# Kernel tuning notes

Hardware: AMD Instinct MI355X
Metric: run time of the kernel (lower is better)

The kernel has to match this reference:

```python
import jax, jax.numpy as jnp
import numpy as np

OBS, ACT, H, O, B = 256, 64, 1024, 8, 4096
ALPHA, GAMMA, ACT_LIMIT = 0.2, 0.99, 1.0
LOG_STD_MIN, LOG_STD_MAX = -20.0, 2.0
D = OBS + ACT + O  # intra-Q input dim


def setup_inputs() -> dict:
    key = jax.random.key(0)
    ks = iter(jax.random.split(key, 64))
    w = lambda shape: (jax.random.normal(next(ks), shape) * 0.05).astype(jnp.float32)
    inp = {}
    inp["state"] = jax.random.normal(next(ks), (B, OBS), jnp.float32)
    inp["action"] = jnp.tanh(jax.random.normal(next(ks), (B, ACT), jnp.float32))
    inp["next_state"] = jax.random.normal(next(ks), (B, OBS), jnp.float32)
    inp["reward"] = jax.random.normal(next(ks), (B, 1), jnp.float32)
    inp["done"] = jnp.zeros((B, 1), jnp.float32)
    inp["noise"] = jax.random.normal(next(ks), (B, ACT), jnp.float32)
    inp["option"] = jax.random.randint(next(ks), (B,), 0, O, jnp.int32)
    # online inter-Q (q1,q2 stacked on leading axis): obs -> H -> H -> O
    inp["interq_W1"], inp["interq_b1"] = w((2, OBS, H)), w((2, H))
    inp["interq_W2"], inp["interq_b2"] = w((2, H, H)), w((2, H))
    inp["interq_W3"], inp["interq_b3"] = w((2, H, O)), w((2, O))
    # target inter-Q
    inp["tinterq_W1"], inp["tinterq_b1"] = w((2, OBS, H)), w((2, H))
    inp["tinterq_W2"], inp["tinterq_b2"] = w((2, H, H)), w((2, H))
    inp["tinterq_W3"], inp["tinterq_b3"] = w((2, H, O)), w((2, O))
    # intra-Q (q1,q2 stacked): [obs,act,onehot] -> H -> H -> 1
    inp["intraq_W1"], inp["intraq_b1"] = w((2, D, H)), w((2, H))
    inp["intraq_W2"], inp["intraq_b2"] = w((2, H, H)), w((2, H))
    inp["intraq_W3"], inp["intraq_b3"] = w((2, H, 1)), w((2, 1))
    # per-option squashed-Gaussian policies: obs -> H -> H -> (mu, log_std)
    inp["pol_W1"], inp["pol_b1"] = w((O, OBS, H)), w((O, H))
    inp["pol_W2"], inp["pol_b2"] = w((O, H, H)), w((O, H))
    inp["pol_Wmu"], inp["pol_bmu"] = w((O, H, ACT)), w((O, ACT))
    inp["pol_Wls"], inp["pol_bls"] = w((O, H, ACT)), w((O, ACT))
    # per-option termination (beta) nets: obs -> H -> 1, sigmoid
    inp["beta_W1"], inp["beta_b1"] = w((O, OBS, H)), w((O, H))
    inp["beta_W2"], inp["beta_b2"] = w((O, H, 1)), w((O, 1))
    return inp


def _mlp2_k(x, W1, b1, W2, b2, W3, b3):
    # x: [B,in], params stacked over leading k -> [k,B,out]
    h = jax.nn.relu(jnp.einsum('bi,kih->kbh', x, W1) + b1[:, None, :])
    h = jax.nn.relu(jnp.einsum('kbh,khg->kbg', h, W2) + b2[:, None, :])
    return jnp.einsum('kbg,kgo->kbo', h, W3) + b3[:, None, :]


def _forward(state, action, next_state, reward, done, noise,
             interq_W1, interq_b1, interq_W2, interq_b2, interq_W3, interq_b3,
             tinterq_W1, tinterq_b1, tinterq_W2, tinterq_b2, tinterq_W3, tinterq_b3,
             intraq_W1, intraq_b1, intraq_W2, intraq_b2, intraq_W3, intraq_b3,
             pol_W1, pol_b1, pol_W2, pol_b2, pol_Wmu, pol_bmu, pol_Wls, pol_bls,
             beta_W1, beta_b1, beta_W2, beta_b2, option):
    idx = jnp.arange(state.shape[0])
    onehot = jax.nn.one_hot(option, O, dtype=state.dtype)
    # intra Q on (state, action, onehot)
    xq = jnp.concatenate([state, action, onehot], axis=-1)  # [B,D]
    q_intra = _mlp2_k(xq, intraq_W1, intraq_b1, intraq_W2, intraq_b2, intraq_W3, intraq_b3)
    q1_intra, q2_intra = q_intra[0], q_intra[1]  # [B,1]
    # option-routed policy: compute all options, gather top-1 (grouped-MoE form)
    h = jax.nn.relu(jnp.einsum('bi,oih->boh', state, pol_W1) + pol_b1)      # [B,O,H]
    h = jax.nn.relu(jnp.einsum('boh,ohg->bog', h, pol_W2) + pol_b2)         # [B,O,H]
    mu = (jnp.einsum('bog,oga->boa', h, pol_Wmu) + pol_bmu)[idx, option]    # [B,ACT]
    ls = (jnp.einsum('bog,oga->boa', h, pol_Wls) + pol_bls)[idx, option]
    ls = jnp.clip(ls, LOG_STD_MIN, LOG_STD_MAX)
    pre = mu + jnp.exp(ls) * noise  # reparameterized pre-tanh action
    LOG2PI = jnp.float32(np.log(2.0 * np.pi))
    logp = jnp.sum(-0.5 * noise**2 - ls - 0.5 * LOG2PI, axis=-1)
    logp = logp - jnp.sum(2.0 * (jnp.log(jnp.float32(2.0)) - pre - jax.nn.softplus(-2.0 * pre)), axis=-1)  # [B]
    current_actions = ACT_LIMIT * jnp.tanh(pre)  # [B,ACT]
    # option-routed termination prob on next_state
    hb = jax.nn.relu(jnp.einsum('bi,oih->boh', next_state, beta_W1) + beta_b1)
    blog = jnp.einsum('boh,oh->bo', hb, beta_W2[..., 0]) + beta_b2[:, 0]
    beta_prob = jax.nn.sigmoid(blog)[idx, option][:, None]  # [B,1]
    # TD target (no-grad in torch)
    q_t = _mlp2_k(next_state, tinterq_W1, tinterq_b1, tinterq_W2, tinterq_b2, tinterq_W3, tinterq_b3)
    q_inter_targ = jnp.minimum(q_t[0], q_t[1])  # [B,O]
    q_cur = q_inter_targ[idx, option][:, None]
    q_on = _mlp2_k(next_state, interq_W1, interq_b1, interq_W2, interq_b2, interq_W3, interq_b3)
    next_opt = jnp.argmax(jnp.minimum(q_on[0], q_on[1]), axis=-1)  # greedy next option
    q_next = q_inter_targ[idx, next_opt][:, None]
    bp = jax.lax.stop_gradient(beta_prob)
    backup = jax.lax.stop_gradient(
        reward + GAMMA * (1.0 - done) * ((1.0 - bp) * q_cur + bp * q_next))
    loss_intra_q = jnp.mean((q1_intra - backup) ** 2) + jnp.mean((q2_intra - backup) ** 2)
    q_pi = jax.lax.stop_gradient(jnp.minimum(q1_intra, q2_intra))[:, 0]
    loss_intra_pi = jnp.mean(ALPHA * logp - q_pi)
    return (loss_intra_q, loss_intra_pi, current_actions, logp, beta_prob)


def reference(state, action, next_state, reward, done, noise,
              interq_W1, interq_b1, interq_W2, interq_b2, interq_W3, interq_b3,
              tinterq_W1, tinterq_b1, tinterq_W2, tinterq_b2, tinterq_W3, tinterq_b3,
              intraq_W1, intraq_b1, intraq_W2, intraq_b2, intraq_W3, intraq_b3,
              pol_W1, pol_b1, pol_W2, pol_b2, pol_Wmu, pol_bmu, pol_Wls, pol_bls,
              beta_W1, beta_b1, beta_W2, beta_b2, option):
    return _forward(state, action, next_state, reward, done, noise,
                    interq_W1, interq_b1, interq_W2, interq_b2, interq_W3, interq_b3,
                    tinterq_W1, tinterq_b1, tinterq_W2, tinterq_b2, tinterq_W3, tinterq_b3,
                    intraq_W1, intraq_b1, intraq_W2, intraq_b2, intraq_W3, intraq_b3,
                    pol_W1, pol_b1, pol_W2, pol_b2, pol_Wmu, pol_bmu, pol_Wls, pol_bls,
                    beta_W1, beta_b1, beta_W2, beta_b2, option)
```

## Files before the change

### kernel.cpp

```cpp
#include <hip/hip_runtime.h>
#include <stdint.h>

#define B_SZ 4096
#define OBS 256
#define ACT 64
#define HID 1024
#define NOPT 8

typedef __attribute__((ext_vector_type(8))) short short8;
typedef __attribute__((ext_vector_type(4))) float floatx4;

constexpr long long OFF_WT_I1 = 0;
constexpr long long OFF_WT_I2 = OFF_WT_I1 + 2LL*1024*256*2;
constexpr long long OFF_WT_T1 = OFF_WT_I2 + 2LL*1024*1024*2;
constexpr long long OFF_WT_T2 = OFF_WT_T1 + 2LL*1024*256*2;
constexpr long long OFF_WT_X1 = OFF_WT_T2 + 2LL*1024*1024*2;
constexpr long long OFF_WT_X2 = OFF_WT_X1 + 2LL*1024*384*2;
constexpr long long OFF_WT_P1 = OFF_WT_X2 + 2LL*1024*1024*2;
constexpr long long OFF_WT_P2 = OFF_WT_P1 + 8LL*1024*256*2;
constexpr long long OFF_WT_ML = OFF_WT_P2 + 8LL*1024*1024*2;
constexpr long long OFF_WT_B1 = OFF_WT_ML + 8LL*128*1024*2;
constexpr long long OFF_XQ    = OFF_WT_B1 + 8LL*1024*256*2;
constexpr long long OFF_NS    = OFF_XQ + 4096LL*384*2;
constexpr long long OFF_AGS   = OFF_NS + 4096LL*256*2;
constexpr long long OFF_AGN   = OFF_AGS + 4224LL*256*2;
constexpr long long OFF_HAX   = OFF_AGN + 4224LL*256*2;
constexpr long long OFF_HAI   = OFF_HAX + 2LL*4096*1024*2;
constexpr long long OFF_HAT   = OFF_HAI + 2LL*4096*1024*2;
constexpr long long OFF_HAP   = OFF_HAT + 2LL*4096*1024*2;
constexpr long long OFF_HAB   = OFF_HAP + 4224LL*1024*2;
constexpr long long OFF_HBP   = OFF_HAB + 4224LL*1024*2;
constexpr long long OFF_QI    = OFF_HBP + 4224LL*1024*2;
constexpr long long OFF_QON   = OFF_QI + 2LL*8*4096*4;
constexpr long long OFF_QT    = OFF_QON + 2LL*8*4096*8*4;
constexpr long long OFF_MULS  = OFF_QT + 2LL*8*4096*8*4;
constexpr long long OFF_PERM  = OFF_MULS + 4224LL*128*4;
constexpr long long OFF_OPTG  = OFF_PERM + 4096LL*4;
constexpr long long OFF_BP    = OFF_OPTG + ((4224LL*4 + 255) & ~255LL);
constexpr long long OFF_LOGP  = OFF_BP + 4096LL*4;
constexpr long long OFF_TILEB = OFF_LOGP + 4096LL*4;
constexpr long long OFF_TILEC = OFF_TILEB + 272LL*64;
constexpr long long OFF_TILED = OFF_TILEC + 232LL*64;
constexpr long long WS_TOTAL  = OFF_TILED + 40LL*64;

struct Tile {
  long long aOff, wOff, cOff;
  int mStart, mEnd, K, nCols, flags, biasSel, biasOff, redSel, redOff, pad0;
};
struct Ptrs { const float* bias[9]; const float* w3[3]; };
struct TrSrcs { const float* p[11]; };

__device__ __forceinline__ unsigned short f2bf(float x){
  union { float f; unsigned u; } v; v.f = x;
  unsigned r = v.u + 0x7fffu + ((v.u >> 16) & 1u);
  return (unsigned short)(r >> 16);
}
__device__ __forceinline__ float bf2f(unsigned short h){
  union { float f; unsigned u; } v; v.u = ((unsigned)h) << 16; return v.f;
}
__device__ __forceinline__ void load16(const void* g, void* l){
  __builtin_amdgcn_global_load_lds((const __attribute__((address_space(1))) void*)g,
                                   (__attribute__((address_space(3))) void*)l, 16, 0, 0);
}

__device__ const int tr_cum[12] = {0,512,2560,3072,5120,5888,7936,9984,18176,18688,19200,21248};
__device__ const int tr_gx[11]  = {8,32,8,32,12,32,8,32,32,32,8};
__device__ const int tr_K[11]   = {256,1024,256,1024,328,1024,256,1024,1024,1024,256};
__device__ const int tr_Kp[11]  = {256,1024,256,1024,384,1024,256,1024,1024,1024,256};
__device__ const int tr_N[11]   = {1024,1024,1024,1024,1024,1024,1024,1024,64,64,1024};
__device__ const long long tr_ws[11] = {256*1024,1024*1024,256*1024,1024*1024,328*1024,1024*1024,256*1024,1024*1024,1024*64,1024*64,256*1024};
__device__ const long long tr_ts[11] = {1024*256,1024*1024,1024*256,1024*1024,1024*384,1024*1024,1024*256,1024*1024,128*1024,128*1024,1024*256};
__device__ const long long tr_dst[11] = {OFF_WT_I1,OFF_WT_I2,OFF_WT_T1,OFF_WT_T2,OFF_WT_X1,OFF_WT_X2,OFF_WT_P1,OFF_WT_P2,OFF_WT_ML,OFF_WT_ML+64LL*1024*2,OFF_WT_B1};

__global__ void k_tr_all(char* __restrict__ wsB, TrSrcs srcs){
  int id = blockIdx.x, j = 0;
  while (id >= tr_cum[j+1]) j++;
  int tloc = id - tr_cum[j];
  int gx = tr_gx[j], gy = tr_N[j] >> 5;
  int per = gx*gy;
  int z = tloc / per, r = tloc % per;
  int kx = r % gx, ny = r / gx;
  int K = tr_K[j], Kpad = tr_Kp[j], N = tr_N[j];
  const float* src = srcs.p[j] + (long long)z * tr_ws[j];
  unsigned short* dst = (unsigned short*)(wsB + tr_dst[j]) + (long long)z * tr_ts[j];
  __shared__ float tile[32][33];
  int k0 = kx*32, n0 = ny*32;
  int tx = threadIdx.x, ty = threadIdx.y;
  #pragma unroll
  for (int i=0;i<4;i++){
    int k = k0 + ty + i*8;
    tile[ty+i*8][tx] = (k < K) ? src[(long long)k*N + n0 + tx] : 0.f;
  }
  __syncthreads();
  #pragma unroll
  for (int i=0;i<4;i++){
    int n = n0 + ty + i*8;
    dst[(long long)n*Kpad + k0 + tx] = f2bf(tile[tx][ty+i*8]);
  }
}

__global__ void k_route(char* __restrict__ wsB, const int* __restrict__ option,
                        float* __restrict__ out){
  __shared__ int cnt[NOPT], off[NOPT+1], cur[NOPT], ctiles[NOPT], toff[NOPT+1];
  int tid = threadIdx.x;
  int* perm = (int*)(wsB + OFF_PERM);
  int* optg = (int*)(wsB + OFF_OPTG);
  Tile* tb = (Tile*)(wsB + OFF_TILEB);
  Tile* tc = (Tile*)(wsB + OFF_TILEC);
  Tile* tdt = (Tile*)(wsB + OFF_TILED);
  if (tid < NOPT) cnt[tid] = 0;
  __syncthreads();
  for (int b = tid; b < B_SZ; b += 256) atomicAdd(&cnt[option[b]], 1);
  __syncthreads();
  if (tid == 0){
    off[0] = 0; toff[0] = 0;
    for (int o=0;o<NOPT;o++){
      off[o+1] = off[o] + cnt[o];
      ctiles[o] = (cnt[o] + 127) >> 7;
      toff[o+1] = toff[o] + ctiles[o];
      cur[o] = off[o];
    }
    out[0] = 0.f; out[1] = 0.f;
  }
  __syncthreads();
  for (int b = tid; b < B_SZ; b += 256){
    int o = option[b];
    int pos = atomicAdd(&cur[o], 1);
    perm[pos] = b; optg[pos] = o;
  }
  __syncthreads();
  if (tid < 192){
    int task = tid/32, mt = tid%32, z = task&1, net = task>>1;
    int ms = mt*128;
    Tile T{};
    T.mStart = ms; T.mEnd = 4096; T.nCols = 1024; T.flags = 0;
    T.redSel = 0; T.redOff = 0;
    if (net==0){ T.K=384; T.aOff = OFF_XQ + (long long)ms*768; T.wOff = OFF_WT_X1 + (long long)z*786432; T.cOff = OFF_HAX + (long long)z*8388608; T.biasSel=0; }
    else if (net==1){ T.K=256; T.aOff = OFF_NS + (long long)ms*512; T.wOff = OFF_WT_I1 + (long long)z*524288; T.cOff = OFF_HAI + (long long)z*8388608; T.biasSel=1; }
    else { T.K=256; T.aOff = OFF_NS + (long long)ms*512; T.wOff = OFF_WT_T1 + (long long)z*524288; T.cOff = OFF_HAT + (long long)z*8388608; T.biasSel=2; }
    T.biasOff = z*1024;
    tb[tid] = T;
    Tile C{};
    C.mStart = ms; C.mEnd = 4096; C.K = 1024; C.nCols = 1024;
    if (net==0){ C.flags=2; C.aOff = OFF_HAX + (long long)z*8388608 + (long long)ms*2048; C.wOff = OFF_WT_X2 + (long long)z*2097152; C.cOff = OFF_QI + (long long)z*131072; C.biasSel=5; C.redSel=0; C.redOff=z*1024; }
    else if (net==1){ C.flags=3; C.aOff = OFF_HAI + (long long)z*8388608 + (long long)ms*2048; C.wOff = OFF_WT_I2 + (long long)z*2097152; C.cOff = OFF_QON + (long long)z*1048576; C.biasSel=6; C.redSel=1; C.redOff=z*8192; }
    else { C.flags=3; C.aOff = OFF_HAT + (long long)z*8388608 + (long long)ms*2048; C.wOff = OFF_WT_T2 + (long long)z*2097152; C.cOff = OFF_QT + (long long)z*1048576; C.biasSel=7; C.redSel=2; C.redOff=z*8192; }
    C.biasOff = z*1024;
    tc[tid] = C;
  }
  if (tid < NOPT){
    int o = tid, base = toff[o], gs = off[o], ge = off[o+1];
    for (int t=0; t<ctiles[o]; t++){
      int ms = gs + t*128;
      Tile P{};
      P.mStart=ms; P.mEnd=ge; P.K=256; P.nCols=1024; P.flags=0;
      P.aOff = OFF_AGS + (long long)ms*512; P.wOff = OFF_WT_P1 + (long long)o*524288;
      P.cOff = OFF_HAP; P.biasSel=3; P.biasOff=o*1024;
      tb[192 + base + t] = P;
      Tile Bt{};
      Bt.mStart=ms; Bt.mEnd=ge; Bt.K=256; Bt.nCols=1024; Bt.flags=0;
      Bt.aOff = OFF_AGN + (long long)ms*512; Bt.wOff = OFF_WT_B1 + (long long)o*524288;
      Bt.cOff = OFF_HAB; Bt.biasSel=4; Bt.biasOff=o*1024;
      tb[232 + base + t] = Bt;
      Tile C2{};
      C2.mStart=ms; C2.mEnd=ge; C2.K=1024; C2.nCols=1024; C2.flags=0;
      C2.aOff = OFF_HAP + (long long)ms*2048; C2.wOff = OFF_WT_P2 + (long long)o*2097152;
      C2.cOff = OFF_HBP; C2.biasSel=8; C2.biasOff=o*1024;
      tc[192 + base + t] = C2;
      Tile M{};
      M.mStart=ms; M.mEnd=ge; M.K=1024; M.nCols=128; M.flags=1;
      M.aOff = OFF_HBP + (long long)ms*2048; M.wOff = OFF_WT_ML + (long long)o*262144;
      M.cOff = OFF_MULS; M.biasSel=-1;
      tdt[base + t] = M;
    }
  }
  __syncthreads();
  int tT = toff[NOPT];
  for (int s = tT + tid; s < 40; s += 256){
    tb[192+s].K = 0; tb[232+s].K = 0; tc[192+s].K = 0; tdt[s].K = 0;
  }
}

__global__ void k_prep(char* __restrict__ wsB, const float* __restrict__ state,
                       const float* __restrict__ action, const float* __restrict__ nstate,
                       const int* __restrict__ option){
  int blk = blockIdx.x, tid = threadIdx.x;
  const int* perm = (const int*)(wsB + OFF_PERM);
  if (blk < 4224){
    unsigned short* agS = (unsigned short*)(wsB + OFF_AGS);
    unsigned short* agN = (unsigned short*)(wsB + OFF_AGN);
    long long o = (long long)blk*256 + tid;
    if (blk < 4096){
      long long src = (long long)perm[blk]*256 + tid;
      agS[o] = f2bf(state[src]); agN[o] = f2bf(nstate[src]);
    } else { agS[o] = 0; agN[o] = 0; }
  } else if (blk < 8320){
    int b = blk - 4224;
    unsigned short* xq = (unsigned short*)(wsB + OFF_XQ);
    for (int c = tid; c < 384; c += 256){
      float v;
      if (c < 256) v = state[(long long)b*256 + c];
      else if (c < 320) v = action[(long long)b*64 + (c-256)];
      else if (c < 328) v = (option[b] == (c-320)) ? 1.f : 0.f;
      else v = 0.f;
      xq[(long long)b*384 + c] = f2bf(v);
    }
  } else {
    long long i = (long long)(blk-8320)*1024 + tid;
    unsigned short* nsb = (unsigned short*)(wsB + OFF_NS);
    #pragma unroll
    for (int k=0;k<4;k++){ nsb[i] = f2bf(nstate[i]); i += 256; }
  }
}

__global__ __launch_bounds__(256, 2)
void k_gemm(char* __restrict__ wsB, long long tileOff, Ptrs ptrs){
  __shared__ unsigned short As[128*64];
  __shared__ unsigned short Bs[256*64];
  Tile t = ((const Tile*)(wsB + tileOff))[blockIdx.y];
  if (t.K == 0) return;
  int n0 = blockIdx.x * 256;
  if (n0 >= t.nCols) return;

  int tid = threadIdx.x;
  int wave = tid >> 6, lane = tid & 63;
  int wm = wave & 1, wn = wave >> 1;
  int quad = lane >> 4, l16 = lane & 15;

  const floatx4 fzero = {0.f,0.f,0.f,0.f};
  floatx4 acc[4][8];
  #pragma unroll
  for (int mi=0;mi<4;mi++)
    #pragma unroll
    for (int ni=0;ni<8;ni++) acc[mi][ni] = fzero;

  long long rowBytes = (long long)t.K*2;
  const char* Abase = wsB + t.aOff;
  const char* Bbase = wsB + t.wOff + (long long)n0*rowBytes;

  int ra0 = tid >> 2, ka0 = (tid & 3) * 16;
  int ra1 = (tid + 256) >> 2, ka1 = ka0;
  char* lA = (char*)As + (long long)tid*16;
  char* lB = (char*)Bs + (long long)tid*16;

  int nkb = t.K >> 6;
  for (int kb = 0; kb < nkb; kb++){
    long long kbb = (long long)kb*128;
    load16(Abase + (long long)ra0*rowBytes + kbb + ka0,      lA);
    load16(Abase + (long long)ra0*rowBytes + kbb + 64 + ka0, lA + 8192);
    load16(Abase + (long long)ra1*rowBytes + kbb + ka1,      lA + 4096);
    load16(Abase + (long long)ra1*rowBytes + kbb + 64 + ka1, lA + 12288);
    #pragma unroll
    for (int j=0;j<4;j++){
      int cb = tid + j*256;
      int rb = cb >> 2, kbo = (cb & 3) * 16;
      load16(Bbase + (long long)rb*rowBytes + kbb + kbo,      lB + j*4096);
      load16(Bbase + (long long)rb*rowBytes + kbb + 64 + kbo, lB + 16384 + j*4096);
    }
    __syncthreads();
    #pragma unroll
    for (int h=0; h<2; h++){
      short8 af[4], bfr[8];
      #pragma unroll
      for (int mi=0;mi<4;mi++)
        af[mi] = *(const short8*)((const char*)As + h*8192 + (wm*64 + mi*16 + l16)*64 + quad*16);
      #pragma unroll
      for (int ni=0;ni<8;ni++)
        bfr[ni] = *(const short8*)((const char*)Bs + h*16384 + (wn*128 + ni*16 + l16)*64 + quad*16);
      #pragma unroll
      for (int mi=0;mi<4;mi++)
        #pragma unroll
        for (int ni=0;ni<8;ni++)
          acc[mi][ni] = __builtin_amdgcn_mfma_f32_16x16x32_bf16(af[mi], bfr[ni], acc[mi][ni], 0, 0, 0);
    }
    __syncthreads();
  }

  if (t.flags <= 1){
    const float* bz = (t.biasSel >= 0) ? (ptrs.bias[t.biasSel] + t.biasOff) : nullptr;
    #pragma unroll
    for (int ni=0;ni<8;ni++){
      int col = n0 + wn*128 + ni*16 + l16;
      if (col >= t.nCols) continue;
      float bval = bz ? bz[col] : 0.f;
      #pragma unroll
      for (int mi=0;mi<4;mi++){
        int rbase = t.mStart + wm*64 + mi*16 + quad*4;
        floatx4 v = acc[mi][ni];
        #pragma unroll
        for (int r=0;r<4;r++){
          int grow = rbase + r;
          if (grow < t.mEnd){
            float x = v[r] + bval;
            if (t.flags == 0){
              x = fmaxf(x, 0.f);
              ((unsigned short*)(wsB + t.cOff))[(long long)grow*t.nCols + col] = f2bf(x);
            } else {
              ((float*)(wsB + t.cOff))[(long long)grow*t.nCols + col] = x;
            }
          }
        }
      }
    }
  } else {
    int NC = (t.flags == 2) ? 1 : 8;
    const float* w3 = ptrs.w3[t.redSel] + t.redOff;
    const float* bz = ptrs.bias[t.biasSel] + t.biasOff;
    int sl = blockIdx.x*2 + wn;
    float* red = (float*)(wsB + t.cOff) + (long long)sl*4096*NC;
    float bv[8]; int colv[8];
    #pragma unroll
    for (int ni=0;ni<8;ni++){ colv[ni] = n0 + wn*128 + ni*16 + l16; bv[ni] = bz[colv[ni]]; }
    #pragma unroll
    for (int mi=0;mi<4;mi++){
      #pragma unroll
      for (int r=0;r<4;r++){
        int row = t.mStart + wm*64 + mi*16 + quad*4 + r;
        float v[8];
        #pragma unroll
        for (int c=0;c<8;c++) v[c] = 0.f;
        #pragma unroll
        for (int ni=0;ni<8;ni++){
          float x = fmaxf(acc[mi][ni][r] + bv[ni], 0.f);
          if (NC == 1) v[0] += x * w3[colv[ni]];
          else {
            #pragma unroll
            for (int c=0;c<8;c++) v[c] += x * w3[colv[ni]*8 + c];
          }
        }
        for (int c=0;c<NC;c++){
          float s = v[c];
          s += __shfl_xor(s,1); s += __shfl_xor(s,2); s += __shfl_xor(s,4); s += __shfl_xor(s,8);
          if (l16 == 0 && row < t.mEnd) red[(long long)row*NC + c] = s;
        }
      }
    }
  }
}

__global__ void k_bp(char* __restrict__ wsB, const float* __restrict__ noise,
                     const float* __restrict__ bmu, const float* __restrict__ bls,
                     const float* __restrict__ beW2, const float* __restrict__ beb2,
                     float* __restrict__ out){
  int job = blockIdx.x*4 + (threadIdx.x >> 6);
  int lane = threadIdx.x & 63;
  const int* perm = (const int*)(wsB + OFF_PERM);
  const int* optg = (const int*)(wsB + OFF_OPTG);
  if (job < B_SZ){
    int i = job, o = optg[i], b = perm[i];
    const float* muls = (const float*)(wsB + OFF_MULS);
    float* logp = (float*)(wsB + OFF_LOGP);
    float mu = muls[(long long)i*128 + lane] + bmu[o*ACT + lane];
    float ls = muls[(long long)i*128 + 64 + lane] + bls[o*ACT + lane];
    ls = fminf(fmaxf(ls, -20.f), 2.f);
    float nv = noise[(long long)b*ACT + lane];
    float pre = mu + expf(ls)*nv;
    out[2 + (long long)b*ACT + lane] = tanhf(pre);
    float xx = -2.f*pre;
    float sp = fmaxf(xx, 0.f) + log1pf(expf(-fabsf(xx)));
    const float LOG2PI = 1.8378770664093453f;
    const float LN2 = 0.6931471805599453f;
    float lp = -0.5f*nv*nv - ls - 0.5f*LOG2PI - 2.f*(LN2 - pre - sp);
    for (int s=32;s;s>>=1) lp += __shfl_xor(lp, s);
    if (lane == 0){ out[2 + (long long)B_SZ*ACT + b] = lp; logp[b] = lp; }
  } else {
    int i = job - B_SZ, o = optg[i], b = perm[i];
    const char* hrow = wsB + OFF_HAB + (long long)i*2048;
    const float* w = beW2 + (long long)o*HID;
    float* bp = (float*)(wsB + OFF_BP);
    short8 v0 = *(const short8*)(hrow + lane*16);
    short8 v1 = *(const short8*)(hrow + 1024 + lane*16);
    float acc = 0.f;
    #pragma unroll
    for (int e=0;e<8;e++){
      acc += bf2f((unsigned short)v0[e]) * w[lane*8 + e];
      acc += bf2f((unsigned short)v1[e]) * w[512 + lane*8 + e];
    }
    for (int s=32;s;s>>=1) acc += __shfl_xor(acc, s);
    if (lane == 0){
      float v = 1.f/(1.f + expf(-(acc + beb2[o])));
      out[2 + (long long)B_SZ*ACT + B_SZ + b] = v; bp[b] = v;
    }
  }
}

__global__ void k_td(const char* __restrict__ wsB, const int* __restrict__ option,
                     const float* __restrict__ reward, const float* __restrict__ done,
                     const float* __restrict__ xb3, const float* __restrict__ ib3,
                     const float* __restrict__ tb3, float* __restrict__ out){
  int b = blockIdx.x*256 + threadIdx.x;
  const float* qiP  = (const float*)(wsB + OFF_QI);
  const float* qonP = (const float*)(wsB + OFF_QON);
  const float* qtP  = (const float*)(wsB + OFF_QT);
  const float* bp   = (const float*)(wsB + OFF_BP);
  const float* logp = (const float*)(wsB + OFF_LOGP);
  float q1 = xb3[0], q2 = xb3[1];
  #pragma unroll
  for (int sl=0; sl<8; sl++){
    q1 += qiP[sl*4096 + b];
    q2 += qiP[32768 + sl*4096 + b];
  }
  float qons[2][8], qts[2][8];
  #pragma unroll
  for (int z=0;z<2;z++)
    #pragma unroll
    for (int o=0;o<8;o++){ qons[z][o] = ib3[z*8+o]; qts[z][o] = tb3[z*8+o]; }
  for (int z=0;z<2;z++){
    for (int sl=0; sl<8; sl++){
      long long base = ((long long)(z*8 + sl)*4096 + b)*8;
      #pragma unroll
      for (int o=0;o<8;o++){ qons[z][o] += qonP[base+o]; qts[z][o] += qtP[base+o]; }
    }
  }
  float qitv[NOPT];
  #pragma unroll
  for (int o=0;o<NOPT;o++) qitv[o] = fminf(qts[0][o], qts[1][o]);
  float qcur = qitv[option[b]];
  float best = -1e30f; int bo = 0;
  #pragma unroll
  for (int o=0;o<NOPT;o++){
    float v = fminf(qons[0][o], qons[1][o]);
    if (v > best){ best = v; bo = o; }
  }
  float qnext = qitv[bo];
  float bpv = bp[b];
  float backup = reward[b] + 0.99f*(1.f - done[b])*((1.f - bpv)*qcur + bpv*qnext);
  float d1 = q1 - backup, d2 = q2 - backup;
  float tq = d1*d1 + d2*d2;
  float qpi = fminf(q1, q2);
  float tp = 0.2f*logp[b] - qpi;
  for (int s=32;s;s>>=1){ tq += __shfl_xor(tq, s); tp += __shfl_xor(tp, s); }
  __shared__ float sq[4], sp2[4];
  int wave = threadIdx.x>>6, lane = threadIdx.x&63;
  if (lane==0){ sq[wave]=tq; sp2[wave]=tp; }
  __syncthreads();
  if (threadIdx.x==0){
    atomicAdd(&out[0], (sq[0]+sq[1]+sq[2]+sq[3])/(float)B_SZ);
    atomicAdd(&out[1], (sp2[0]+sp2[1]+sp2[2]+sp2[3])/(float)B_SZ);
  }
}

extern "C" void kernel_launch(void* const* d_in, const int* in_sizes, int n_in,
                              void* d_out, int out_size, void* d_ws, size_t ws_size,
                              hipStream_t stream){
  const float* state  = (const float*)d_in[0];
  const float* action = (const float*)d_in[1];
  const float* nstate = (const float*)d_in[2];
  const float* reward = (const float*)d_in[3];
  const float* done   = (const float*)d_in[4];
  const float* noise  = (const float*)d_in[5];
  const int*   option = (const int*)d_in[6];
  const float* iq_W1 = (const float*)d_in[7];  const float* iq_b1 = (const float*)d_in[8];
  const float* iq_W2 = (const float*)d_in[9];  const float* iq_b2 = (const float*)d_in[10];
  const float* iq_W3 = (const float*)d_in[11]; const float* iq_b3 = (const float*)d_in[12];
  const float* tq_W1 = (const float*)d_in[13]; const float* tq_b1 = (const float*)d_in[14];
  const float* tq_W2 = (const float*)d_in[15]; const float* tq_b2 = (const float*)d_in[16];
  const float* tq_W3 = (const float*)d_in[17]; const float* tq_b3 = (const float*)d_in[18];
  const float* xw_W1 = (const float*)d_in[19]; const float* xw_b1 = (const float*)d_in[20];
  const float* xw_W2 = (const float*)d_in[21]; const float* xw_b2 = (const float*)d_in[22];
  const float* xw_W3 = (const float*)d_in[23]; const float* xw_b3 = (const float*)d_in[24];
  const float* p_W1 = (const float*)d_in[25];  const float* p_b1 = (const float*)d_in[26];
  const float* p_W2 = (const float*)d_in[27];  const float* p_b2 = (const float*)d_in[28];
  const float* p_Wmu = (const float*)d_in[29]; const float* p_bmu = (const float*)d_in[30];
  const float* p_Wls = (const float*)d_in[31]; const float* p_bls = (const float*)d_in[32];
  const float* be_W1 = (const float*)d_in[33]; const float* be_b1 = (const float*)d_in[34];
  const float* be_W2 = (const float*)d_in[35]; const float* be_b2 = (const float*)d_in[36];
  float* out = (float*)d_out;
  char* wsB = (char*)d_ws;
  if ((long long)ws_size < WS_TOTAL) return;

  TrSrcs trs;
  trs.p[0]=iq_W1; trs.p[1]=iq_W2; trs.p[2]=tq_W1; trs.p[3]=tq_W2; trs.p[4]=xw_W1;
  trs.p[5]=xw_W2; trs.p[6]=p_W1; trs.p[7]=p_W2; trs.p[8]=p_Wmu; trs.p[9]=p_Wls; trs.p[10]=be_W1;
  Ptrs ptrs;
  ptrs.bias[0]=xw_b1; ptrs.bias[1]=iq_b1; ptrs.bias[2]=tq_b1; ptrs.bias[3]=p_b1; ptrs.bias[4]=be_b1;
  ptrs.bias[5]=xw_b2; ptrs.bias[6]=iq_b2; ptrs.bias[7]=tq_b2; ptrs.bias[8]=p_b2;
  ptrs.w3[0]=xw_W3; ptrs.w3[1]=iq_W3; ptrs.w3[2]=tq_W3;

  k_route<<<1, 256, 0, stream>>>(wsB, option, out);
  k_tr_all<<<21248, dim3(32,8), 0, stream>>>(wsB, trs);
  k_prep<<<9344, 256, 0, stream>>>(wsB, state, action, nstate, option);
  k_gemm<<<dim3(4,272), 256, 0, stream>>>(wsB, OFF_TILEB, ptrs);
  k_gemm<<<dim3(4,232), 256, 0, stream>>>(wsB, OFF_TILEC, ptrs);
  k_gemm<<<dim3(1,40), 256, 0, stream>>>(wsB, OFF_TILED, ptrs);
  k_bp<<<2048, 256, 0, stream>>>(wsB, noise, p_bmu, p_bls, be_W2, be_b2, out);
  k_td<<<B_SZ/256, 256, 0, stream>>>(wsB, option, reward, done, xw_b3, iq_b3, tq_b3, out);
}
```

Baseline: 508.1 us.

## Prefetch next K-tile into registers to overlap global loads with MFMA

Replaces the direct global-to-LDS loads in the GEMM main loop with register prefetch. The next K block is read into registers while the current block's MFMAs run, then written to LDS after a barrier. This is meant to hide global memory latency behind compute. It costs extra VGPRs on top of a 128-register accumulator, which may lower occupancy, and adds a second barrier per iteration.

```diff
diff --git a/kernel.cpp b/kernel.cpp
--- a/kernel.cpp
+++ b/kernel.cpp
@@ -9,6 +9,7 @@
 
 typedef __attribute__((ext_vector_type(8))) short short8;
 typedef __attribute__((ext_vector_type(4))) float floatx4;
+typedef __attribute__((ext_vector_type(4))) unsigned int u32x4;
 
 constexpr long long OFF_WT_I1 = 0;
 constexpr long long OFF_WT_I2 = OFF_WT_I1 + 2LL*1024*256*2;
@@ -58,10 +59,6 @@
 __device__ __forceinline__ float bf2f(unsigned short h){
   union { float f; unsigned u; } v; v.u = ((unsigned)h) << 16; return v.f;
 }
-__device__ __forceinline__ void load16(const void* g, void* l){
-  __builtin_amdgcn_global_load_lds((const __attribute__((address_space(1))) void*)g,
-                                   (__attribute__((address_space(3))) void*)l, 16, 0, 0);
-}
 
 __device__ const int tr_cum[12] = {0,512,2560,3072,5120,5888,7936,9984,18176,18688,19200,21248};
 __device__ const int tr_gx[11]  = {8,32,8,32,12,32,8,32,32,32,8};
@@ -239,25 +236,43 @@
   const char* Bbase = wsB + t.wOff + (long long)n0*rowBytes;
 
   int ra0 = tid >> 2, ka0 = (tid & 3) * 16;
-  int ra1 = (tid + 256) >> 2, ka1 = ka0;
-  char* lA = (char*)As + (long long)tid*16;
-  char* lB = (char*)Bs + (long long)tid*16;
+  int ra1 = ra0 + 64;
+  const char* gA0 = Abase + (long long)ra0*rowBytes + ka0;
+  const char* gA1 = Abase + (long long)ra1*rowBytes + ka0;
+  const char* gBp[4];
+  #pragma unroll
+  for (int j=0;j<4;j++){
+    int rb = (tid >> 2) + j*64;
+    gBp[j] = Bbase + (long long)rb*rowBytes + ka0;
+  }
+
+  u32x4 pA[4], pB[8];
+  #define PREFETCH(KBB) { \
+    long long _kb = (KBB); \
+    pA[0] = *(const u32x4*)(gA0 + _kb);      pA[1] = *(const u32x4*)(gA0 + _kb + 64); \
+    pA[2] = *(const u32x4*)(gA1 + _kb);      pA[3] = *(const u32x4*)(gA1 + _kb + 64); \
+    _Pragma("unroll") \
+    for (int j=0;j<4;j++){ \
+      pB[2*j]   = *(const u32x4*)(gBp[j] + _kb); \
+      pB[2*j+1] = *(const u32x4*)(gBp[j] + _kb + 64); \
+    } }
+  #define STAGE() { \
+    *(u32x4*)((char*)As + tid*16)         = pA[0]; \
+    *(u32x4*)((char*)As + 8192 + tid*16)  = pA[1]; \
+    *(u32x4*)((char*)As + 4096 + tid*16)  = pA[2]; \
+    *(u32x4*)((char*)As + 12288 + tid*16) = pA[3]; \
+    _Pragma("unroll") \
+    for (int j=0;j<4;j++){ \
+      *(u32x4*)((char*)Bs + j*4096 + tid*16)         = pB[2*j]; \
+      *(u32x4*)((char*)Bs + 16384 + j*4096 + tid*16) = pB[2*j+1]; \
+    } }
 
   int nkb = t.K >> 6;
+  PREFETCH(0);
+  STAGE();
+  __syncthreads();
   for (int kb = 0; kb < nkb; kb++){
-    long long kbb = (long long)kb*128;
-    load16(Abase + (long long)ra0*rowBytes + kbb + ka0,      lA);
-    load16(Abase + (long long)ra0*rowBytes + kbb + 64 + ka0, lA + 8192);
-    load16(Abase + (long long)ra1*rowBytes + kbb + ka1,      lA + 4096);
-    load16(Abase + (long long)ra1*rowBytes + kbb + 64 + ka1, lA + 12288);
-    #pragma unroll
-    for (int j=0;j<4;j++){
-      int cb = tid + j*256;
-      int rb = cb >> 2, kbo = (cb & 3) * 16;
-      load16(Bbase + (long long)rb*rowBytes + kbb + kbo,      lB + j*4096);
-      load16(Bbase + (long long)rb*rowBytes + kbb + 64 + kbo, lB + 16384 + j*4096);
-    }
-    __syncthreads();
+    if (kb + 1 < nkb) PREFETCH((long long)(kb+1)*128);
     #pragma unroll
     for (int h=0; h<2; h++){
       short8 af[4], bfr[8];
@@ -274,7 +289,13 @@
           acc[mi][ni] = __builtin_amdgcn_mfma_f32_16x16x32_bf16(af[mi], bfr[ni], acc[mi][ni], 0, 0, 0);
     }
     __syncthreads();
-  }
+    if (kb + 1 < nkb){
+      STAGE();
+      __syncthreads();
+    }
+  }
+  #undef PREFETCH
+  #undef STAGE
 
   if (t.flags <= 1){
     const float* bz = (t.biasSel >= 0) ? (ptrs.bias[t.biasSel] + t.biasOff) : nullptr;
```

New measurement: 501.5 us. Within noise of the previous version (-1.3%).
